# Kernel optimization log

Hardware: AMD Instinct MI355X
Metric: run time of the kernel (lower is better)

Reference implementation:

```python
import jax, jax.numpy as jnp
import numpy as np

N_NODES = 50000


def _sage_conv(x, src, dst, Wl, Wr, b):
    # PyG SAGEConv (aggr='mean'): out = lin_l(mean_{j in N(i)} x_j) + lin_r(x_i)
    msgs = x[src]                                              # [E, d] gather
    s = jax.ops.segment_sum(msgs, dst, num_segments=N_NODES)   # [N, d]
    cnt = jax.ops.segment_sum(jnp.ones((src.shape[0], 1), x.dtype), dst,
                              num_segments=N_NODES)            # [N, 1]
    agg = s / jnp.maximum(cnt, 1.0)                            # mean, 0 if no nbrs
    return agg @ Wl.T + x @ Wr.T + b


def setup_inputs() -> dict:
    key = jax.random.key(0)
    ks = jax.random.split(key, 12)
    in_dim, h = 128, 128
    E, P = 500000, 200000
    x = jax.random.normal(ks[0], (N_NODES, in_dim), dtype=jnp.float32)
    edge_index = jax.random.randint(ks[1], (2, E), 0, N_NODES)
    pairs = jax.random.randint(ks[2], (P, 2), 0, N_NODES)
    def lin(k, fan_out, fan_in):
        bound = 1.0 / np.sqrt(fan_in)
        return jax.random.uniform(k, (fan_out, fan_in), jnp.float32, -bound, bound)
    return {
        "x": x, "edge_index": edge_index, "pairs": pairs,
        "Wl1": lin(ks[3], h, in_dim), "Wr1": lin(ks[4], h, in_dim),
        "b1": jnp.zeros((h,), jnp.float32),
        "Wl2": lin(ks[5], h, h), "Wr2": lin(ks[6], h, h),
        "b2": jnp.zeros((h,), jnp.float32),
        "W3": lin(ks[7], h, 2 * h), "b3": jnp.zeros((h,), jnp.float32),
        "W4": lin(ks[8], 1, h), "b4": jnp.zeros((1,), jnp.float32),
    }


def reference(x, edge_index, pairs, Wl1, Wr1, b1, Wl2, Wr2, b2, W3, b3, W4, b4):
    src, dst = edge_index[0], edge_index[1]
    h1 = jax.nn.relu(_sage_conv(x, src, dst, Wl1, Wr1, b1))    # [N, h]
    h2 = jax.nn.relu(_sage_conv(h1, src, dst, Wl2, Wr2, b2))   # [N, h]
    a = h2[pairs[:, 0]]                                        # [P, h]
    b = h2[pairs[:, 1]]                                        # [P, h]
    z = jnp.concatenate([a, b], axis=1)                        # [P, 2h]
    s = jax.nn.relu(z @ W3.T + b3) @ W4.T + b4                 # [P, 1]
    return jax.nn.sigmoid(s).squeeze(-1)                       # [P]
```

## Files before the change

### kernel.cpp

```cpp
#include <hip/hip_runtime.h>
#include <math.h>

#define N_NODES 50000
#define E_EDGES 500000
#define P_PAIRS 200000
#define MAX_DEG 64

#define NB        196
#define EB        2048
#define EPT       8
#define SORT_BLKS 245

typedef __bf16    bf16x8 __attribute__((ext_vector_type(8)));
typedef _Float16  f16x8  __attribute__((ext_vector_type(8)));
typedef float     f32x4  __attribute__((ext_vector_type(4)));


#define CONV_BLKS 1563
#define PREP_BLKS 128

__global__ __launch_bounds__(256) void pre_k(
        const float* __restrict__ x, __bf16* __restrict__ xb,
        const int* __restrict__ dst,
        int* __restrict__ bucketCnt, int* __restrict__ blockBase,
        const float* __restrict__ Wl1, const float* __restrict__ Wr1,
        const float* __restrict__ Wl2, const float* __restrict__ Wr2,
        const float* __restrict__ W3,
        __bf16* __restrict__ P1, __bf16* __restrict__ P2, __bf16* __restrict__ P4) {
    __shared__ int cnt[NB];
    int b = blockIdx.x, t = threadIdx.x;
    if (b < SORT_BLKS) {
        if (t < NB) cnt[t] = 0;
        __syncthreads();
        int ebase = b * EB;
        #pragma unroll
        for (int i = 0; i < EPT; ++i) {
            int e = ebase + i * 256 + t;
            if (e < E_EDGES) atomicAdd(&cnt[dst[e] >> 8], 1);
        }
        __syncthreads();
        if (t < NB) blockBase[b * NB + t] = atomicAdd(&bucketCnt[t], cnt[t]);
    } else if (b < SORT_BLKS + CONV_BLKS) {
        int i0 = (b - SORT_BLKS) * 1024 + t;
        #pragma unroll
        for (int k = 0; k < 4; ++k) {
            int i = i0 + k * 256;
            if (i < N_NODES * 128 / 4) {
                float4 v = ((const float4*)x)[i];
                __bf16* o = xb + (size_t)i * 4;
                o[0] = (__bf16)v.x; o[1] = (__bf16)v.y; o[2] = (__bf16)v.z; o[3] = (__bf16)v.w;
            }
        }
    } else {
        int i = (b - SORT_BLKS - CONV_BLKS) * 256 + t;
        int lane = (i >> 3) & 63;
        int j = i & 7;
        int kq = (lane >> 4) * 8 + j;
        {
            int kt = i >> 12, nt = (i >> 9) & 7;
            int n = nt * 16 + (lane & 15);
            int k = kt * 32 + kq;
            P1[i] = (__bf16)((k < 128) ? Wl1[n * 128 + k] : Wr1[n * 128 + (k - 128)]);
            P2[i] = (__bf16)((k < 128) ? Wl2[n * 128 + k] : Wr2[n * 128 + (k - 128)]);
        }
        {
            int kt = i >> 13, nt = (i >> 9) & 15;
            int n = nt * 16 + (lane & 15);
            int k = kt * 32 + kq;
            P4[i] = (__bf16)((n < 128) ? W3[n * 256 + k] : W3[(n - 128) * 256 + 128 + k]);
        }
    }
}


__global__ __launch_bounds__(256) void place_k(const int* __restrict__ src,
                                               const int* __restrict__ dst,
                                               const int* __restrict__ bucketCnt,
                                               const int* __restrict__ blockBase,
                                               unsigned* __restrict__ edgebuf) {
    __shared__ int cnt[256];
    __shared__ int buf[256];
    __shared__ int sbase[NB];
    __shared__ int gbase[NB];
    __shared__ int cur[NB];
    __shared__ unsigned sortbuf[EB];
    __shared__ unsigned char bktof[EB];
    int blk = blockIdx.x, t = threadIdx.x;

    int bv = (t < NB) ? bucketCnt[t] : 0;
    buf[t] = bv;
    __syncthreads();
    for (int off = 1; off < 256; off <<= 1) {
        int xv = (t >= off) ? buf[t - off] : 0;
        __syncthreads();
        buf[t] += xv;
        __syncthreads();
    }
    if (t < NB) gbase[t] = (buf[t] - bv) + blockBase[blk * NB + t];
    cnt[t] = 0;
    if (t < NB) cur[t] = 0;
    __syncthreads();

    unsigned packed[EPT];
    int bk[EPT];
    int ebase = blk * EB;
    #pragma unroll
    for (int i = 0; i < EPT; ++i) {
        int e = ebase + i * 256 + t;
        if (e < E_EDGES) {
            int d = dst[e];
            packed[i] = ((unsigned)d << 16) | (unsigned)src[e];
            bk[i] = d >> 8;
            atomicAdd(&cnt[bk[i]], 1);
        } else bk[i] = -1;
    }
    __syncthreads();

    int v = cnt[t];
    buf[t] = v;
    __syncthreads();
    for (int off = 1; off < 256; off <<= 1) {
        int xv = (t >= off) ? buf[t - off] : 0;
        __syncthreads();
        buf[t] += xv;
        __syncthreads();
    }
    if (t < NB) sbase[t] = buf[t] - v;
    __syncthreads();

    #pragma unroll
    for (int i = 0; i < EPT; ++i) {
        if (bk[i] >= 0) {
            int p = sbase[bk[i]] + atomicAdd(&cur[bk[i]], 1);
            sortbuf[p] = packed[i];
            bktof[p] = (unsigned char)bk[i];
        }
    }
    __syncthreads();

    int nE = E_EDGES - ebase; if (nE > EB) nE = EB;
    for (int i = t; i < nE; i += 256) {
        int bb = bktof[i];
        edgebuf[gbase[bb] + (i - sbase[bb])] = sortbuf[i];
    }
}


__global__ __launch_bounds__(256) void slots_k(const unsigned* __restrict__ edgebuf,
                                               const int* __restrict__ bucketCnt,
                                               unsigned short* __restrict__ slots,
                                               int* __restrict__ deg) {
    __shared__ unsigned short srow[256 * MAX_DEG];
    __shared__ int cur[256];
    __shared__ int buf[256];
    __shared__ int sc[2];
    int b = blockIdx.x, t = threadIdx.x;

    int bv = (t < NB) ? bucketCnt[t] : 0;
    buf[t] = bv;
    cur[t] = 0;
    __syncthreads();
    for (int off = 1; off < 256; off <<= 1) {
        int xv = (t >= off) ? buf[t - off] : 0;
        __syncthreads();
        buf[t] += xv;
        __syncthreads();
    }
    if (t == b) { sc[0] = buf[t] - bv; sc[1] = bv; }
    __syncthreads();
    int base = sc[0], n = sc[1];

    for (int i = t; i < n; i += 256) {
        unsigned p = edgebuf[base + i];
        int dl = (p >> 16) & 255;
        int pos = atomicAdd(&cur[dl], 1);
        if (pos < MAX_DEG) srow[dl * MAX_DEG + pos] = (unsigned short)(p & 0xFFFFu);
    }
    __syncthreads();
    unsigned* sl32 = (unsigned*)slots;
    const unsigned* sr32 = (const unsigned*)srow;
    int gbase32 = b * 8192;
    for (int i = t; i < 8192; i += 256) {
        int node = b * 256 + (i >> 5);
        if (node < N_NODES) sl32[gbase32 + i] = sr32[i];
    }
    int node = b * 256 + t;
    if (node < N_NODES) deg[node] = cur[t];
}


__global__ __launch_bounds__(256) void agg1_k(const __bf16* __restrict__ feat,
                                              const int* __restrict__ deg_a,
                                              const unsigned short* __restrict__ slots,
                                              __bf16* __restrict__ agg) {
    int n = blockIdx.x * 4 + (threadIdx.x >> 6);
    if (n >= N_NODES) return;
    int lane = threadIdx.x & 63;
    int slot = lane >> 4, l = lane & 15;
    int deg = deg_a[n];
    int nit = (deg < MAX_DEG) ? deg : MAX_DEG;

    int ed = (lane < nit) ? (int)slots[n * MAX_DEG + lane] : 0;

    float s[8];
    #pragma unroll
    for (int e = 0; e < 8; ++e) s[e] = 0.f;

    int trips = (nit + 3) >> 2;
    int it = slot;
    int k = 0;
    for (; k + 1 < trips; k += 2, it += 8) {
        int sn0 = __builtin_amdgcn_ds_bpermute(it << 2, ed);
        int sn1 = __builtin_amdgcn_ds_bpermute((it + 4) << 2, ed);
        bf16x8 v0 = *(const bf16x8*)(feat + (size_t)sn0 * 128 + l * 8);
        bf16x8 v1 = *(const bf16x8*)(feat + (size_t)sn1 * 128 + l * 8);
        if (it < nit) {
            #pragma unroll
            for (int e = 0; e < 8; ++e) s[e] += (float)v0[e];
        }
        if (it + 4 < nit) {
            #pragma unroll
            for (int e = 0; e < 8; ++e) s[e] += (float)v1[e];
        }
    }
    if (k < trips) {
        int sn = __builtin_amdgcn_ds_bpermute(it << 2, ed);
        bf16x8 v = *(const bf16x8*)(feat + (size_t)sn * 128 + l * 8);
        if (it < nit) {
            #pragma unroll
            for (int e = 0; e < 8; ++e) s[e] += (float)v[e];
        }
    }

    #pragma unroll
    for (int e = 0; e < 8; ++e) {
        s[e] += __shfl_xor(s[e], 16, 64);
        s[e] += __shfl_xor(s[e], 32, 64);
    }

    if (slot == 0) {
        float inv = 1.0f / fmaxf((float)deg, 1.0f);
        bf16x8 o;
        #pragma unroll
        for (int e = 0; e < 8; ++e) o[e] = (__bf16)(s[e] * inv);
        *(bf16x8*)(agg + (size_t)n * 128 + l * 8) = o;
    }
}


__global__ __launch_bounds__(256) void layer_mfma_k(const __bf16* __restrict__ agg,
                                                    const __bf16* __restrict__ feat,
                                                    const __bf16* __restrict__ wpack,
                                                    const float* __restrict__ bias,
                                                    __bf16* __restrict__ out) {
    int wave = threadIdx.x >> 6;
    int lane = threadIdx.x & 63;
    int m = lane & 15, quad = lane >> 4;
    int rbase = blockIdx.x * 64 + wave * 16;
    int r0 = rbase + m; if (r0 > N_NODES - 1) r0 = N_NODES - 1;

    f32x4 acc[8];
    #pragma unroll
    for (int nt = 0; nt < 8; ++nt) acc[nt] = (f32x4)0.f;

    #pragma unroll
    for (int kt = 0; kt < 8; ++kt) {
        const __bf16* src = (kt < 4) ? agg : feat;
        int ko = (kt & 3) * 32 + quad * 8;
        bf16x8 a0 = *(const bf16x8*)(src + (size_t)r0 * 128 + ko);
        const __bf16* wb = wpack + (size_t)kt * 4096 + lane * 8;
        #pragma unroll
        for (int nt = 0; nt < 8; ++nt) {
            bf16x8 b = *(const bf16x8*)(wb + nt * 512);
            acc[nt] = __builtin_amdgcn_mfma_f32_16x16x32_bf16(a0, b, acc[nt], 0, 0, 0);
        }
    }

    #pragma unroll
    for (int r = 0; r < 4; ++r) {
        int row = rbase + quad * 4 + r;
        if (row < N_NODES) {
            #pragma unroll
            for (int nt = 0; nt < 8; ++nt) {
                float v = acc[nt][r] + bias[nt * 16 + m];
                out[(size_t)row * 128 + nt * 16 + m] = (__bf16)fmaxf(v, 0.f);
            }
        }
    }
}


__global__ __launch_bounds__(256) void layer2uv_k(const __bf16* __restrict__ agg,
                                                  const __bf16* __restrict__ feat,
                                                  const __bf16* __restrict__ wpack,
                                                  const float* __restrict__ bias,
                                                  const __bf16* __restrict__ wpack4,
                                                  _Float16* __restrict__ UV) {
    __shared__ __bf16 sh[4][16][136];
    int wave = threadIdx.x >> 6;
    int lane = threadIdx.x & 63;
    int m = lane & 15, q = lane >> 4;
    int rbase = blockIdx.x * 64 + wave * 16;
    int r0 = rbase + m; if (r0 > N_NODES - 1) r0 = N_NODES - 1;

    f32x4 acc[8];
    #pragma unroll
    for (int nt = 0; nt < 8; ++nt) acc[nt] = (f32x4)0.f;

    #pragma unroll
    for (int kt = 0; kt < 8; ++kt) {
        const __bf16* src = (kt < 4) ? agg : feat;
        int ko = (kt & 3) * 32 + q * 8;
        bf16x8 a0 = *(const bf16x8*)(src + (size_t)r0 * 128 + ko);
        const __bf16* wb = wpack + (size_t)kt * 4096 + lane * 8;
        #pragma unroll
        for (int nt = 0; nt < 8; ++nt) {
            bf16x8 b = *(const bf16x8*)(wb + nt * 512);
            acc[nt] = __builtin_amdgcn_mfma_f32_16x16x32_bf16(a0, b, acc[nt], 0, 0, 0);
        }
    }

    #pragma unroll
    for (int rr = 0; rr < 4; ++rr)
        #pragma unroll
        for (int nt = 0; nt < 8; ++nt) {
            float v = acc[nt][rr] + bias[nt * 16 + m];
            sh[wave][q * 4 + rr][nt * 16 + m] = (__bf16)fmaxf(v, 0.f);
        }

    f32x4 acc2[16];
    #pragma unroll
    for (int nt = 0; nt < 16; ++nt) acc2[nt] = (f32x4)0.f;

    #pragma unroll
    for (int kt = 0; kt < 4; ++kt) {
        bf16x8 a = *(const bf16x8*)&sh[wave][m][kt * 32 + q * 8];
        const __bf16* wb = wpack4 + (size_t)kt * 8192 + lane * 8;
        #pragma unroll
        for (int nt = 0; nt < 16; ++nt) {
            bf16x8 b = *(const bf16x8*)(wb + nt * 512);
            acc2[nt] = __builtin_amdgcn_mfma_f32_16x16x32_bf16(a, b, acc2[nt], 0, 0, 0);
        }
    }

    #pragma unroll
    for (int rr = 0; rr < 4; ++rr) {
        int row = rbase + q * 4 + rr;
        if (row < N_NODES) {
            #pragma unroll
            for (int nt = 0; nt < 16; ++nt)
                UV[(size_t)row * 256 + nt * 16 + m] = (_Float16)acc2[nt][rr];
        }
    }
}


__global__ __launch_bounds__(256) void pair_ep_k(const _Float16* __restrict__ UV,
                                                 const int* __restrict__ pairs,
                                                 const float* __restrict__ b3,
                                                 const float* __restrict__ W4,
                                                 const float* __restrict__ b4,
                                                 float* __restrict__ out) {
    int t = threadIdx.x;
    int g = t >> 4, l = t & 15;
    int base = blockIdx.x * 64;

    float4 b3a = *(const float4*)(b3 + l * 8);
    float4 b3b = *(const float4*)(b3 + l * 8 + 4);
    float4 w4a = *(const float4*)(W4 + l * 8);
    float4 w4b = *(const float4*)(W4 + l * 8 + 4);
    float bb[8] = {b3a.x, b3a.y, b3a.z, b3a.w, b3b.x, b3b.y, b3b.z, b3b.w};
    float ww[8] = {w4a.x, w4a.y, w4a.z, w4a.w, w4b.x, w4b.y, w4b.z, w4b.w};
    float b4s = b4[0];

    int2 pr[4];
    #pragma unroll
    for (int i = 0; i < 4; ++i) pr[i] = ((const int2*)pairs)[base + i * 16 + g];

    f16x8 ua[4], vb[4];
    #pragma unroll
    for (int i = 0; i < 4; ++i) {
        ua[i] = *(const f16x8*)(UV + (size_t)pr[i].x * 256 + l * 8);
        vb[i] = *(const f16x8*)(UV + (size_t)pr[i].y * 256 + 128 + l * 8);
    }

    #pragma unroll
    for (int i = 0; i < 4; ++i) {
        float p = 0.f;
        #pragma unroll
        for (int e = 0; e < 8; ++e)
            p += fmaxf((float)ua[i][e] + (float)vb[i][e] + bb[e], 0.f) * ww[e];
        #pragma unroll
        for (int s = 1; s < 16; s <<= 1) p += __shfl_xor(p, s, 64);
        if (l == 0)
            out[base + i * 16 + g] = 1.0f / (1.0f + expf(-(p + b4s)));
    }
}


extern "C" void kernel_launch(void* const* d_in, const int* in_sizes, int n_in,
                              void* d_out, int out_size, void* d_ws, size_t ws_size,
                              hipStream_t stream) {
    const float* x   = (const float*)d_in[0];
    const int*   ei  = (const int*)d_in[1];
    const int*   prs = (const int*)d_in[2];
    const float* Wl1 = (const float*)d_in[3];
    const float* Wr1 = (const float*)d_in[4];
    const float* b1  = (const float*)d_in[5];
    const float* Wl2 = (const float*)d_in[6];
    const float* Wr2 = (const float*)d_in[7];
    const float* b2  = (const float*)d_in[8];
    const float* W3  = (const float*)d_in[9];
    const float* b3  = (const float*)d_in[10];
    const float* W4  = (const float*)d_in[11];
    const float* b4  = (const float*)d_in[12];
    float* out = (float*)d_out;

    const int* srcv = ei;
    const int* dstv = ei + E_EDGES;

    char* ws = (char*)d_ws;
    size_t off = 0;
    auto alloc = [&](size_t bytes) -> void* {
        void* p = ws + off;
        off = (off + bytes + 255) & ~(size_t)255;
        return p;
    };
    int*            bucketCnt  = (int*)alloc(sizeof(int) * NB);
    int*            blockBase  = (int*)alloc(sizeof(int) * SORT_BLKS * NB);
    unsigned*       edgebuf    = (unsigned*)alloc(sizeof(unsigned) * E_EDGES);
    int*            deg        = (int*)alloc(sizeof(int) * N_NODES);
    unsigned short* slots      = (unsigned short*)alloc(sizeof(unsigned short) * (size_t)N_NODES * MAX_DEG + 512);
    __bf16*   P1     = (__bf16*)alloc(sizeof(__bf16) * 32768);
    __bf16*   P2     = (__bf16*)alloc(sizeof(__bf16) * 32768);
    __bf16*   P4     = (__bf16*)alloc(sizeof(__bf16) * 32768);
    __bf16*   xb     = (__bf16*)alloc(sizeof(__bf16) * (size_t)N_NODES * 128);
    __bf16*   aggb   = (__bf16*)alloc(sizeof(__bf16) * (size_t)N_NODES * 128);
    __bf16*   h1b    = (__bf16*)alloc(sizeof(__bf16) * (size_t)N_NODES * 128);
    _Float16* UV     = (_Float16*)alloc(sizeof(_Float16) * (size_t)N_NODES * 256);
    (void)ws_size; (void)in_sizes; (void)n_in; (void)out_size;

    hipMemsetAsync(bucketCnt, 0, sizeof(int) * NB, stream);

    pre_k<<<SORT_BLKS + CONV_BLKS + PREP_BLKS, 256, 0, stream>>>(
        x, xb, dstv, bucketCnt, blockBase, Wl1, Wr1, Wl2, Wr2, W3, P1, P2, P4);
    place_k<<<SORT_BLKS, 256, 0, stream>>>(srcv, dstv, bucketCnt, blockBase, edgebuf);
    slots_k<<<NB, 256, 0, stream>>>(edgebuf, bucketCnt, slots, deg);

    agg1_k<<<(N_NODES + 3) / 4, 256, 0, stream>>>(xb, deg, slots, aggb);
    layer_mfma_k<<<(N_NODES + 63) / 64, 256, 0, stream>>>(aggb, xb, P1, b1, h1b);
    agg1_k<<<(N_NODES + 3) / 4, 256, 0, stream>>>(h1b, deg, slots, aggb);
    layer2uv_k<<<(N_NODES + 63) / 64, 256, 0, stream>>>(aggb, h1b, P2, b2, P4, UV);
    pair_ep_k<<<P_PAIRS / 64, 256, 0, stream>>>(UV, prs, b3, W4, b4, out);
}
```

Baseline: 218.0 us.

## Fuse neighbor aggregation into SAGE layer MFMA kernels via shared-memory tiles

```diff
diff --git a/kernel.cpp b/kernel.cpp
--- a/kernel.cpp
+++ b/kernel.cpp
@@ -12,6 +12,7 @@
 #define SORT_BLKS 245
 
 typedef __bf16    bf16x8 __attribute__((ext_vector_type(8)));
+typedef __bf16    bf16x4 __attribute__((ext_vector_type(4)));
 typedef _Float16  f16x8  __attribute__((ext_vector_type(8)));
 typedef float     f32x4  __attribute__((ext_vector_type(4)));
 
@@ -47,8 +48,10 @@
             int i = i0 + k * 256;
             if (i < N_NODES * 128 / 4) {
                 float4 v = ((const float4*)x)[i];
-                __bf16* o = xb + (size_t)i * 4;
-                o[0] = (__bf16)v.x; o[1] = (__bf16)v.y; o[2] = (__bf16)v.z; o[3] = (__bf16)v.w;
+                bf16x4 o;
+                o[0] = (__bf16)v.x; o[1] = (__bf16)v.y;
+                o[2] = (__bf16)v.z; o[3] = (__bf16)v.w;
+                *(bf16x4*)(xb + (size_t)i * 4) = o;
             }
         }
     } else {
@@ -177,103 +180,111 @@
         if (pos < MAX_DEG) srow[dl * MAX_DEG + pos] = (unsigned short)(p & 0xFFFFu);
     }
     __syncthreads();
-    unsigned* sl32 = (unsigned*)slots;
-    const unsigned* sr32 = (const unsigned*)srow;
-    int gbase32 = b * 8192;
-    for (int i = t; i < 8192; i += 256) {
-        int node = b * 256 + (i >> 5);
-        if (node < N_NODES) sl32[gbase32 + i] = sr32[i];
+    const int4* sr16 = (const int4*)srow;
+    int4* sl16 = (int4*)slots;
+    int gbase16 = b * 2048;
+    for (int i = t; i < 2048; i += 256) {
+        int node = b * 256 + (i >> 3);
+        if (node < N_NODES) sl16[gbase16 + i] = sr16[i];
     }
     int node = b * 256 + t;
     if (node < N_NODES) deg[node] = cur[t];
 }
 
 
-__global__ __launch_bounds__(256) void agg1_k(const __bf16* __restrict__ feat,
-                                              const int* __restrict__ deg_a,
-                                              const unsigned short* __restrict__ slots,
-                                              __bf16* __restrict__ agg) {
-    int n = blockIdx.x * 4 + (threadIdx.x >> 6);
-    if (n >= N_NODES) return;
-    int lane = threadIdx.x & 63;
+__device__ __forceinline__ void agg_tile(const __bf16* __restrict__ feat,
+                                         const int* __restrict__ deg_a,
+                                         const unsigned short* __restrict__ slots,
+                                         int rbase, int lane,
+                                         __bf16 (* __restrict__ shrow)[136]) {
     int slot = lane >> 4, l = lane & 15;
-    int deg = deg_a[n];
-    int nit = (deg < MAX_DEG) ? deg : MAX_DEG;
-
-    int ed = (lane < nit) ? (int)slots[n * MAX_DEG + lane] : 0;
-
-    float s[8];
-    #pragma unroll
-    for (int e = 0; e < 8; ++e) s[e] = 0.f;
-
-    int trips = (nit + 3) >> 2;
-    int it = slot;
-    int k = 0;
-    for (; k + 1 < trips; k += 2, it += 8) {
-        int sn0 = __builtin_amdgcn_ds_bpermute(it << 2, ed);
-        int sn1 = __builtin_amdgcn_ds_bpermute((it + 4) << 2, ed);
-        bf16x8 v0 = *(const bf16x8*)(feat + (size_t)sn0 * 128 + l * 8);
-        bf16x8 v1 = *(const bf16x8*)(feat + (size_t)sn1 * 128 + l * 8);
-        if (it < nit) {
+    int dn = rbase + (lane & 15); if (dn > N_NODES - 1) dn = N_NODES - 1;
+    int dv = deg_a[dn];
+    int edv[16];
+    #pragma unroll
+    for (int i = 0; i < 16; ++i) {
+        int n = rbase + i; if (n > N_NODES - 1) n = N_NODES - 1;
+        edv[i] = (int)slots[(size_t)n * MAX_DEG + lane];
+    }
+    #pragma unroll
+    for (int i = 0; i < 16; ++i) {
+        int deg = __shfl(dv, i, 64);
+        int nit = (deg < MAX_DEG) ? deg : MAX_DEG;
+        float s[8];
+        #pragma unroll
+        for (int e = 0; e < 8; ++e) s[e] = 0.f;
+        int trips = (nit + 3) >> 2;
+        int it = slot, k = 0;
+        for (; k + 1 < trips; k += 2, it += 8) {
+            int sn0 = __builtin_amdgcn_ds_bpermute(it << 2, edv[i]);
+            int sn1 = __builtin_amdgcn_ds_bpermute((it + 4) << 2, edv[i]);
+            bf16x8 v0 = *(const bf16x8*)(feat + (size_t)sn0 * 128 + l * 8);
+            bf16x8 v1 = *(const bf16x8*)(feat + (size_t)sn1 * 128 + l * 8);
+            if (it < nit) {
+                #pragma unroll
+                for (int e = 0; e < 8; ++e) s[e] += (float)v0[e];
+            }
+            if (it + 4 < nit) {
+                #pragma unroll
+                for (int e = 0; e < 8; ++e) s[e] += (float)v1[e];
+            }
+        }
+        if (k < trips) {
+            int sn = __builtin_amdgcn_ds_bpermute(it << 2, edv[i]);
+            bf16x8 v = *(const bf16x8*)(feat + (size_t)sn * 128 + l * 8);
+            if (it < nit) {
+                #pragma unroll
+                for (int e = 0; e < 8; ++e) s[e] += (float)v[e];
+            }
+        }
+        #pragma unroll
+        for (int e = 0; e < 8; ++e) {
+            s[e] += __shfl_xor(s[e], 16, 64);
+            s[e] += __shfl_xor(s[e], 32, 64);
+        }
+        if (slot == 0) {
+            float inv = 1.0f / fmaxf((float)deg, 1.0f);
+            bf16x8 o;
             #pragma unroll
-            for (int e = 0; e < 8; ++e) s[e] += (float)v0[e];
-        }
-        if (it + 4 < nit) {
-            #pragma unroll
-            for (int e = 0; e < 8; ++e) s[e] += (float)v1[e];
-        }
-    }
-    if (k < trips) {
-        int sn = __builtin_amdgcn_ds_bpermute(it << 2, ed);
-        bf16x8 v = *(const bf16x8*)(feat + (size_t)sn * 128 + l * 8);
-        if (it < nit) {
-            #pragma unroll
-            for (int e = 0; e < 8; ++e) s[e] += (float)v[e];
-        }
-    }
-
-    #pragma unroll
-    for (int e = 0; e < 8; ++e) {
-        s[e] += __shfl_xor(s[e], 16, 64);
-        s[e] += __shfl_xor(s[e], 32, 64);
-    }
-
-    if (slot == 0) {
-        float inv = 1.0f / fmaxf((float)deg, 1.0f);
-        bf16x8 o;
-        #pragma unroll
-        for (int e = 0; e < 8; ++e) o[e] = (__bf16)(s[e] * inv);
-        *(bf16x8*)(agg + (size_t)n * 128 + l * 8) = o;
-    }
-}
-
-
-__global__ __launch_bounds__(256) void layer_mfma_k(const __bf16* __restrict__ agg,
-                                                    const __bf16* __restrict__ feat,
-                                                    const __bf16* __restrict__ wpack,
-                                                    const float* __restrict__ bias,
-                                                    __bf16* __restrict__ out) {
+            for (int e = 0; e < 8; ++e) o[e] = (__bf16)(s[e] * inv);
+            *(bf16x8*)&shrow[i][l * 8] = o;
+        }
+    }
+}
+
+
+__global__ __launch_bounds__(256) void fused_l1_k(const __bf16* __restrict__ feat,
+                                                  const int* __restrict__ deg_a,
+                                                  const unsigned short* __restrict__ slots,
+                                                  const __bf16* __restrict__ wpack,
+                                                  const float* __restrict__ bias,
+                                                  __bf16* __restrict__ out) {
+    __shared__ __bf16 shA[4][16][136];
     int wave = threadIdx.x >> 6;
     int lane = threadIdx.x & 63;
     int m = lane & 15, quad = lane >> 4;
     int rbase = blockIdx.x * 64 + wave * 16;
+
+    agg_tile(feat, deg_a, slots, rbase, lane, shA[wave]);
+
     int r0 = rbase + m; if (r0 > N_NODES - 1) r0 = N_NODES - 1;
-
     f32x4 acc[8];
     #pragma unroll
     for (int nt = 0; nt < 8; ++nt) acc[nt] = (f32x4)0.f;
 
     #pragma unroll
     for (int kt = 0; kt < 8; ++kt) {
-        const __bf16* src = (kt < 4) ? agg : feat;
-        int ko = (kt & 3) * 32 + quad * 8;
-        bf16x8 a0 = *(const bf16x8*)(src + (size_t)r0 * 128 + ko);
+        bf16x8 a0;
+        if (kt < 4) a0 = *(const bf16x8*)&shA[wave][m][kt * 32 + quad * 8];
+        else        a0 = *(const bf16x8*)(feat + (size_t)r0 * 128 + (kt & 3) * 32 + quad * 8);
         const __bf16* wb = wpack + (size_t)kt * 4096 + lane * 8;
+        __builtin_amdgcn_s_setprio(1);
         #pragma unroll
         for (int nt = 0; nt < 8; ++nt) {
             bf16x8 b = *(const bf16x8*)(wb + nt * 512);
             acc[nt] = __builtin_amdgcn_mfma_f32_16x16x32_bf16(a0, b, acc[nt], 0, 0, 0);
         }
+        __builtin_amdgcn_s_setprio(0);
     }
 
     #pragma unroll
@@ -290,34 +301,40 @@
 }
 
 
-__global__ __launch_bounds__(256) void layer2uv_k(const __bf16* __restrict__ agg,
-                                                  const __bf16* __restrict__ feat,
+__global__ __launch_bounds__(256) void fused_l2_k(const __bf16* __restrict__ feat,
+                                                  const int* __restrict__ deg_a,
+                                                  const unsigned short* __restrict__ slots,
                                                   const __bf16* __restrict__ wpack,
                                                   const float* __restrict__ bias,
                                                   const __bf16* __restrict__ wpack4,
                                                   _Float16* __restrict__ UV) {
-    __shared__ __bf16 sh[4][16][136];
+    __shared__ __bf16 shA[4][16][136];
+    __shared__ __bf16 shH[4][16][136];
     int wave = threadIdx.x >> 6;
     int lane = threadIdx.x & 63;
     int m = lane & 15, q = lane >> 4;
     int rbase = blockIdx.x * 64 + wave * 16;
+
+    agg_tile(feat, deg_a, slots, rbase, lane, shA[wave]);
+
     int r0 = rbase + m; if (r0 > N_NODES - 1) r0 = N_NODES - 1;
-
     f32x4 acc[8];
     #pragma unroll
     for (int nt = 0; nt < 8; ++nt) acc[nt] = (f32x4)0.f;
 
     #pragma unroll
     for (int kt = 0; kt < 8; ++kt) {
-        const __bf16* src = (kt < 4) ? agg : feat;
-        int ko = (kt & 3) * 32 + q * 8;
-        bf16x8 a0 = *(const bf16x8*)(src + (size_t)r0 * 128 + ko);
+        bf16x8 a0;
+        if (kt < 4) a0 = *(const bf16x8*)&shA[wave][m][kt * 32 + q * 8];
+        else        a0 = *(const bf16x8*)(feat + (size_t)r0 * 128 + (kt & 3) * 32 + q * 8);
         const __bf16* wb = wpack + (size_t)kt * 4096 + lane * 8;
+        __builtin_amdgcn_s_setprio(1);
         #pragma unroll
         for (int nt = 0; nt < 8; ++nt) {
             bf16x8 b = *(const bf16x8*)(wb + nt * 512);
             acc[nt] = __builtin_amdgcn_mfma_f32_16x16x32_bf16(a0, b, acc[nt], 0, 0, 0);
         }
+        __builtin_amdgcn_s_setprio(0);
     }
 
     #pragma unroll
@@ -325,7 +342,7 @@
         #pragma unroll
         for (int nt = 0; nt < 8; ++nt) {
             float v = acc[nt][rr] + bias[nt * 16 + m];
-            sh[wave][q * 4 + rr][nt * 16 + m] = (__bf16)fmaxf(v, 0.f);
+            shH[wave][q * 4 + rr][nt * 16 + m] = (__bf16)fmaxf(v, 0.f);
         }
 
     f32x4 acc2[16];
@@ -334,13 +351,15 @@
 
     #pragma unroll
     for (int kt = 0; kt < 4; ++kt) {
-        bf16x8 a = *(const bf16x8*)&sh[wave][m][kt * 32 + q * 8];
+        bf16x8 a = *(const bf16x8*)&shH[wave][m][kt * 32 + q * 8];
         const __bf16* wb = wpack4 + (size_t)kt * 8192 + lane * 8;
+        __builtin_amdgcn_s_setprio(1);
         #pragma unroll
         for (int nt = 0; nt < 16; ++nt) {
             bf16x8 b = *(const bf16x8*)(wb + nt * 512);
             acc2[nt] = __builtin_amdgcn_mfma_f32_16x16x32_bf16(a, b, acc2[nt], 0, 0, 0);
         }
+        __builtin_amdgcn_s_setprio(0);
     }
 
     #pragma unroll
@@ -435,7 +454,6 @@
     __bf16*   P2     = (__bf16*)alloc(sizeof(__bf16) * 32768);
     __bf16*   P4     = (__bf16*)alloc(sizeof(__bf16) * 32768);
     __bf16*   xb     = (__bf16*)alloc(sizeof(__bf16) * (size_t)N_NODES * 128);
-    __bf16*   aggb   = (__bf16*)alloc(sizeof(__bf16) * (size_t)N_NODES * 128);
     __bf16*   h1b    = (__bf16*)alloc(sizeof(__bf16) * (size_t)N_NODES * 128);
     _Float16* UV     = (_Float16*)alloc(sizeof(_Float16) * (size_t)N_NODES * 256);
     (void)ws_size; (void)in_sizes; (void)n_in; (void)out_size;
@@ -447,9 +465,7 @@
     place_k<<<SORT_BLKS, 256, 0, stream>>>(srcv, dstv, bucketCnt, blockBase, edgebuf);
     slots_k<<<NB, 256, 0, stream>>>(edgebuf, bucketCnt, slots, deg);
 
-    agg1_k<<<(N_NODES + 3) / 4, 256, 0, stream>>>(xb, deg, slots, aggb);
-    layer_mfma_k<<<(N_NODES + 63) / 64, 256, 0, stream>>>(aggb, xb, P1, b1, h1b);
-    agg1_k<<<(N_NODES + 3) / 4, 256, 0, stream>>>(h1b, deg, slots, aggb);
-    layer2uv_k<<<(N_NODES + 63) / 64, 256, 0, stream>>>(aggb, h1b, P2, b2, P4, UV);
+    fused_l1_k<<<(N_NODES + 63) / 64, 256, 0, stream>>>(xb, deg, slots, P1, b1, h1b);
+    fused_l2_k<<<(N_NODES + 63) / 64, 256, 0, stream>>>(h1b, deg, slots, P2, b2, P4, UV);
     pair_ep_k<<<P_PAIRS / 64, 256, 0, stream>>>(UV, prs, b3, W4, b4, out);
 }
```

After: 233.4 us. 7.1% more time.
